# Performance work log

Measured on AMD Instinct MI355X. Metric: run time of the kernel, lower is better.

Reference implementation:

```python
import math
import jax, jax.numpy as jnp
import numpy as np

B, N, D = 4, 1024, 512
HEADS, K = 8, 3
DH = D // HEADS
SMAX, SMIN, ALPHA_S = 0.2, 0.8, 3.0


def setup_inputs() -> dict:
    key = jax.random.key(0)
    ks = jax.random.split(key, 6)
    X = jax.random.normal(ks[0], (B, N, D), dtype=jnp.float32)
    # per-head GraphConstructor temperature (init 1.0 in torch)
    temperature = jnp.ones((HEADS,), dtype=jnp.float32)
    # per-head, per-hop filter weights: [HEADS, K+1, DH, DH]
    W_filt = jax.random.normal(ks[1], (HEADS, K + 1, DH, DH), dtype=jnp.float32) / math.sqrt(DH)
    # per-head hop mixing coefficients (random so output is non-trivial)
    alpha = jax.random.normal(ks[2], (HEADS, K + 1), dtype=jnp.float32) * 0.5
    W_proj = jax.random.normal(ks[3], (D, D), dtype=jnp.float32) / math.sqrt(D)
    b_proj = jnp.zeros((D,), dtype=jnp.float32)
    return {"X": X, "temperature": temperature, "W_filt": W_filt, "alpha": alpha,
            "W_proj": W_proj, "b_proj": b_proj, "layer_idx": 1, "L": 4}


def reference(X, temperature, W_filt, alpha, W_proj, b_proj, layer_idx, L):
    b, n, d = X.shape
    Xh = X.reshape(b, n, HEADS, DH).transpose(0, 2, 1, 3)  # [B,H,N,DH]

    # sparsity schedule -> static top-k size
    sparsity = SMIN + (SMAX - SMIN) * math.exp(-ALPHA_S * layer_idx / L)
    k_val = max(1, int((1.0 - sparsity) * n))

    tau = jnp.clip(temperature, 0.1, 5.0)  # [H]
    scale = math.sqrt(DH)
    # per-head attention scores: [B,H,N,N]
    S = jnp.einsum('bhnd,bhmd->bhnm', Xh, Xh) / (scale * tau[None, :, None, None])

    if k_val < n:
        thresh = jax.lax.top_k(S, k_val)[0][..., -1:]  # k-th largest per row
        S = jnp.where(S < thresh, -jnp.inf, S)
    A = jax.nn.softmax(S, axis=-1)  # row-stochastic sparse-pattern adjacency

    # K-hop polynomial filter, all heads at once
    P = Xh
    H = alpha[None, :, 0, None, None] * jnp.einsum('bhnd,hde->bhne', P, W_filt[:, 0])
    for k in range(1, K + 1):
        P = jnp.einsum('bhnm,bhmd->bhnd', A, P)
        H = H + alpha[None, :, k, None, None] * jnp.einsum('bhnd,hde->bhne', P, W_filt[:, k])

    out = H.transpose(0, 2, 1, 3).reshape(b, n, d)  # concat heads
    return out @ W_proj.T + b_proj
```

## Files before the change

### kernel.cpp

```cpp
#include <hip/hip_runtime.h>
#include <math.h>

#define Nq   1024
#define Dq   512
#define Hq   8
#define KH   3
#define DHq  64
#define NBH  32

typedef __attribute__((ext_vector_type(8))) __bf16 bf16x8;
typedef __attribute__((ext_vector_type(4))) float f32x4;

#define LDA 136
#define LDW 72


__device__ __forceinline__ unsigned short f2bf(float f) {
    unsigned int u = __float_as_uint(f);
    u += 0x7FFFu + ((u >> 16) & 1u);
    return (unsigned short)(u >> 16);
}
__device__ __forceinline__ float bf2f(unsigned short b) {
    return __uint_as_float(((unsigned int)b) << 16);
}
__device__ __forceinline__ unsigned key16(unsigned int b) {
    return (b & 0x8000u) ? (0xFFFFu & ~b) : (b | 0x8000u);
}
__device__ __forceinline__ uint2 pack4(float4 v) {
    return make_uint2((unsigned)f2bf(v.x) | ((unsigned)f2bf(v.y) << 16),
                      (unsigned)f2bf(v.z) | ((unsigned)f2bf(v.w) << 16));
}
__device__ __forceinline__ f32x4 fzero() { f32x4 z = {0.f, 0.f, 0.f, 0.f}; return z; }



__global__ __launch_bounds__(256) void xcast_kernel(const float* __restrict__ X,
                                                    unsigned short* __restrict__ Xn,
                                                    unsigned short* __restrict__ Xt,
                                                    const float* __restrict__ Wf,
                                                    const float* __restrict__ Wp,
                                                    unsigned short* __restrict__ WtB,
                                                    unsigned short* __restrict__ WpB) {
    int tid = threadIdx.x;
    if (blockIdx.y == 32) {
        int bx = blockIdx.x;
#pragma unroll
        for (int mm = 0; mm < 2; ++mm) {
            int m = bx * 2 + mm;
            for (int u = tid; u < 4096; u += 256) {
                int d = u >> 6, e = u & 63;
                WtB[m * 4096 + e * 64 + d] = f2bf(Wf[m * 4096 + d * 64 + e]);
            }
        }
        for (int u = tid; u < 32 * 128; u += 256) {
            int r = bx * 32 + (u >> 7), c4 = (u & 127) << 2;
            float4 v = *(const float4*)&Wp[(size_t)r * Dq + c4];
            *(uint2*)&WpB[(size_t)r * Dq + c4] = pack4(v);
        }
        return;
    }
    __shared__ float T[64][68];
    int bh = blockIdx.y, b = bh >> 3, h = bh & 7;
    int n0 = blockIdx.x << 6;
    const float* Xg = X + ((size_t)b * Nq + n0) * Dq + h * DHq;
#pragma unroll
    for (int u = 0; u < 4; ++u) {
        int idx = tid + (u << 8);
        int r = idx >> 4, c4 = (idx & 15) << 2;
        float4 v = *(const float4*)&Xg[(size_t)r * Dq + c4];
        *(uint2*)&Xn[((size_t)bh * Nq + n0 + r) * DHq + c4] = pack4(v);
        T[c4 + 0][r] = v.x; T[c4 + 1][r] = v.y; T[c4 + 2][r] = v.z; T[c4 + 3][r] = v.w;
    }
    __syncthreads();
#pragma unroll
    for (int u = 0; u < 4; ++u) {
        int idx = tid + (u << 8);
        int d = idx >> 4, n4 = (idx & 15) << 2;
        float4 v = make_float4(T[d][n4], T[d][n4 + 1], T[d][n4 + 2], T[d][n4 + 3]);
        *(uint2*)&Xt[((size_t)bh * DHq + d) * Nq + n0 + n4] = pack4(v);
    }
}

__global__ __launch_bounds__(256) void score_mfma(const unsigned short* __restrict__ Xn,
                                                  const float* __restrict__ temperature,
                                                  unsigned short* __restrict__ Sbf) {
    __shared__ unsigned short Xi[64 * LDW], Xj[64 * LDW];
    int tid = threadIdx.x, lane = tid & 63, w = tid >> 6;
    int bh = blockIdx.z, i0 = blockIdx.y << 6, j0 = blockIdx.x << 6;
    const unsigned short* Xb = Xn + (size_t)bh * Nq * DHq;
    {
        int row = tid >> 3, o = (tid & 7) << 3;
#pragma unroll
        for (int u = 0; u < 2; ++u) {
            int r = row + (u << 5);
            *(uint4*)&Xi[r * LDW + o] = *(const uint4*)&Xb[(size_t)(i0 + r) * DHq + o];
            *(uint4*)&Xj[r * LDW + o] = *(const uint4*)&Xb[(size_t)(j0 + r) * DHq + o];
        }
    }
    __syncthreads();
    f32x4 acc[4] = {fzero(), fzero(), fzero(), fzero()};
    int brow = lane & 15, ko = (lane >> 4) << 3;
    const unsigned short* Afr = &Xi[((w << 4) + brow) * LDW + ko];
#pragma unroll
    for (int ks = 0; ks < 2; ++ks) {
        bf16x8 af = *(const bf16x8*)(Afr + (ks << 5));
#pragma unroll
        for (int nt = 0; nt < 4; ++nt) {
            bf16x8 bfv = *(const bf16x8*)&Xj[((nt << 4) + brow) * LDW + (ks << 5) + ko];
            acc[nt] = __builtin_amdgcn_mfma_f32_16x16x32_bf16(af, bfv, acc[nt], 0, 0, 0);
        }
    }
    float tau = fminf(fmaxf(temperature[bh & 7], 0.1f), 5.0f);
    float inv = 1.0f / (8.0f * tau);
    int nrow = (w << 4) + ((lane >> 4) << 2);
    unsigned short* Sp = Sbf + ((size_t)bh * Nq + i0 + nrow) * Nq + j0;
#pragma unroll
    for (int nt = 0; nt < 4; ++nt)
#pragma unroll
        for (int r = 0; r < 4; ++r)
            Sp[(size_t)r * Nq + (nt << 4) + brow] = f2bf(acc[nt][r] * inv);
}

__global__ __launch_bounds__(256) void topk_softmax_kernel(unsigned short* __restrict__ Sbf,
                                                           const int* __restrict__ layer_idx,
                                                           const int* __restrict__ Lptr) {
    int tid = threadIdx.x;
    int w = tid >> 6, lane = tid & 63;
    unsigned short* Srow = Sbf + ((size_t)blockIdx.x * 4 + w) * Nq;
    uint4 q0 = ((const uint4*)Srow)[lane * 2];
    uint4 q1 = ((const uint4*)Srow)[lane * 2 + 1];
    float v[16]; unsigned int k16[16];
    {
        unsigned int ww[8] = {q0.x, q0.y, q0.z, q0.w, q1.x, q1.y, q1.z, q1.w};
#pragma unroll
        for (int i = 0; i < 8; ++i) {
            unsigned lo16 = ww[i] & 0xFFFFu, hi16 = ww[i] >> 16;
            v[2 * i]       = __uint_as_float(lo16 << 16);
            v[2 * i + 1]   = __uint_as_float(hi16 << 16);
            k16[2 * i]     = key16(lo16);
            k16[2 * i + 1] = key16(hi16);
        }
    }

    double sp = 0.8 + (0.2 - 0.8) * exp(-3.0 * (double)layer_idx[0] / (double)Lptr[0]);
    int kv = (int)((1.0 - sp) * (double)Nq);
    if (kv < 1) kv = 1;

    float m = v[0];
#pragma unroll
    for (int i = 1; i < 16; ++i) m = fmaxf(m, v[i]);
#pragma unroll
    for (int off = 32; off; off >>= 1) m = fmaxf(m, __shfl_xor(m, off));
    unsigned int maxk = key16(__float_as_uint(m) >> 16);

    unsigned int tk = 0;
    if (kv < Nq) {
        unsigned int lo = 0;
#pragma unroll
        for (int bit = 15; bit >= 0; --bit) {
            unsigned int t = lo | (1u << bit);
            if (t > maxk) continue;
            int cnt = 0;
#pragma unroll
            for (int i = 0; i < 16; ++i)
                cnt += (int)__popcll(__ballot(k16[i] >= t));
            if (cnt >= kv) lo = t;
        }
        tk = lo;
    }

    float sum = 0.f;
#pragma unroll
    for (int i = 0; i < 16; ++i) {
        float e = (k16[i] >= tk) ? __expf(v[i] - m) : 0.0f;
        v[i] = e; sum += e;
    }
#pragma unroll
    for (int off = 32; off; off >>= 1) sum += __shfl_xor(sum, off);
    float is = 1.0f / sum;
    unsigned int ow[8];
#pragma unroll
    for (int i = 0; i < 8; ++i)
        ow[i] = (unsigned)f2bf(v[2 * i] * is) | ((unsigned)f2bf(v[2 * i + 1] * is) << 16);
    ((uint4*)Srow)[lane * 2]     = make_uint4(ow[0], ow[1], ow[2], ow[3]);
    ((uint4*)Srow)[lane * 2 + 1] = make_uint4(ow[4], ow[5], ow[6], ow[7]);
}

__global__ __launch_bounds__(256) void apf_mfma(const unsigned short* __restrict__ Abf,
                                                const unsigned short* __restrict__ Ptin,
                                                unsigned short* __restrict__ Ptout, int writeP,
                                                const unsigned short* __restrict__ Xn,
                                                const unsigned short* __restrict__ WtB,
                                                const float* __restrict__ alpha,
                                                unsigned short* __restrict__ HaccB, int khop) {
    __shared__ unsigned short A_lds[2][64 * LDA];
    __shared__ unsigned short P_lds[2][64 * LDA];
    int tid = threadIdx.x, lane = tid & 63, w = tid >> 6;
    int bh = blockIdx.y, b = bh >> 3, h = bh & 7;
    int i0 = blockIdx.x << 6;
    const unsigned short* Ag = Abf + ((size_t)bh * Nq + i0) * Nq;
    const unsigned short* Pg = Ptin + (size_t)bh * DHq * Nq;
    int r0 = tid >> 4, oo = (tid & 15) << 3;

    uint4 ra[4], rp[4];
#pragma unroll
    for (int u = 0; u < 4; ++u) {
        ra[u] = *(const uint4*)&Ag[(size_t)(r0 + (u << 4)) * Nq + oo];
        rp[u] = *(const uint4*)&Pg[(size_t)(r0 + (u << 4)) * Nq + oo];
    }
#pragma unroll
    for (int u = 0; u < 4; ++u) {
        *(uint4*)&A_lds[0][(r0 + (u << 4)) * LDA + oo] = ra[u];
        *(uint4*)&P_lds[0][(r0 + (u << 4)) * LDA + oo] = rp[u];
    }
    __syncthreads();

    f32x4 acc[4] = {fzero(), fzero(), fzero(), fzero()};
    int brow = lane & 15, g = lane >> 4, ko = g << 3;
    int cur = 0;

    for (int kt = 0; kt < 8; ++kt) {
        if (kt < 7) {
            int j = (kt + 1) << 7;
#pragma unroll
            for (int u = 0; u < 4; ++u) {
                ra[u] = *(const uint4*)&Ag[(size_t)(r0 + (u << 4)) * Nq + j + oo];
                rp[u] = *(const uint4*)&Pg[(size_t)(r0 + (u << 4)) * Nq + j + oo];
            }
        }
        const unsigned short* Afr = &A_lds[cur][((w << 4) + brow) * LDA + ko];
#pragma unroll
        for (int ks = 0; ks < 4; ++ks) {
            bf16x8 af = *(const bf16x8*)(Afr + (ks << 5));
#pragma unroll
            for (int nt = 0; nt < 4; ++nt) {
                bf16x8 bfv = *(const bf16x8*)&P_lds[cur][((nt << 4) + brow) * LDA + (ks << 5) + ko];
                acc[nt] = __builtin_amdgcn_mfma_f32_16x16x32_bf16(af, bfv, acc[nt], 0, 0, 0);
            }
        }
        if (kt < 7) {
#pragma unroll
            for (int u = 0; u < 4; ++u) {
                *(uint4*)&A_lds[cur ^ 1][(r0 + (u << 4)) * LDA + oo] = ra[u];
                *(uint4*)&P_lds[cur ^ 1][(r0 + (u << 4)) * LDA + oo] = rp[u];
            }
        }
        __syncthreads();
        cur ^= 1;
    }

    int nrow = (w << 4) + (g << 2);
    int dcol = brow;
    if (writeP) {
#pragma unroll
        for (int nt = 0; nt < 4; ++nt) {
            uint2 pk = make_uint2(
                (unsigned)f2bf(acc[nt][0]) | ((unsigned)f2bf(acc[nt][1]) << 16),
                (unsigned)f2bf(acc[nt][2]) | ((unsigned)f2bf(acc[nt][3]) << 16));
            *(uint2*)&Ptout[(size_t)bh * DHq * Nq + (size_t)((nt << 4) + dcol) * Nq + i0 + nrow] = pk;
        }
    }
    unsigned short* PnL = &A_lds[0][0];
#pragma unroll
    for (int nt = 0; nt < 4; ++nt)
#pragma unroll
        for (int r = 0; r < 4; ++r)
            PnL[(nrow + r) * LDW + (nt << 4) + dcol] = f2bf(acc[nt][r]);

    const unsigned short* Wk = WtB + (size_t)(h * (KH + 1) + khop) * DHq * DHq;
    f32x4 hacc[4] = {fzero(), fzero(), fzero(), fzero()};
    f32x4 hacc0[4] = {fzero(), fzero(), fzero(), fzero()};
#pragma unroll
    for (int ks = 0; ks < 2; ++ks) {
        bf16x8 pf = *(const bf16x8*)&PnL[((w << 4) + brow) * LDW + (ks << 5) + ko];
#pragma unroll
        for (int nt = 0; nt < 4; ++nt) {
            bf16x8 wf = *(const bf16x8*)&Wk[(size_t)((nt << 4) + brow) * DHq + (ks << 5) + ko];
            hacc[nt] = __builtin_amdgcn_mfma_f32_16x16x32_bf16(pf, wf, hacc[nt], 0, 0, 0);
        }
    }
    if (khop == 1) {
        const unsigned short* W0 = WtB + (size_t)(h * (KH + 1)) * DHq * DHq;
        const unsigned short* Xb = Xn + ((size_t)bh * Nq + i0) * DHq;
        int arow = (w << 4) + brow;
#pragma unroll
        for (int ks = 0; ks < 2; ++ks) {
            bf16x8 xf = *(const bf16x8*)&Xb[(size_t)arow * DHq + (ks << 5) + ko];
#pragma unroll
            for (int nt = 0; nt < 4; ++nt) {
                bf16x8 wf = *(const bf16x8*)&W0[(size_t)((nt << 4) + brow) * DHq + (ks << 5) + ko];
                hacc0[nt] = __builtin_amdgcn_mfma_f32_16x16x32_bf16(xf, wf, hacc0[nt], 0, 0, 0);
            }
        }
    }
    float av = alpha[h * (KH + 1) + khop];
    unsigned short* Ho = HaccB + ((size_t)b * Nq + i0 + nrow) * Dq + h * DHq;
    if (khop == 1) {
        float a0 = alpha[h * (KH + 1)];
#pragma unroll
        for (int nt = 0; nt < 4; ++nt)
#pragma unroll
            for (int r = 0; r < 4; ++r)
                Ho[(size_t)r * Dq + (nt << 4) + brow] = f2bf(a0 * hacc0[nt][r] + av * hacc[nt][r]);
    } else {
#pragma unroll
        for (int nt = 0; nt < 4; ++nt)
#pragma unroll
            for (int r = 0; r < 4; ++r) {
                unsigned short* p = Ho + (size_t)r * Dq + (nt << 4) + brow;
                *p = f2bf(bf2f(*p) + av * hacc[nt][r]);
            }
    }
}

__global__ __launch_bounds__(256) void proj_mfma(const unsigned short* __restrict__ HaccB,
                                                 const unsigned short* __restrict__ WpB,
                                                 const float* __restrict__ bp,
                                                 float* __restrict__ out) {
    __shared__ unsigned short Hl[64 * LDA], Wl[64 * LDA];
    int tid = threadIdx.x, lane = tid & 63, w = tid >> 6;
    int i0 = blockIdx.y << 6, j0 = blockIdx.x << 6;
    int brow = lane & 15, ko = (lane >> 4) << 3;
    f32x4 acc[4] = {fzero(), fzero(), fzero(), fzero()};
    for (int kt = 0; kt < 4; ++kt) {
#pragma unroll
        for (int u = 0; u < 4; ++u) {
            int idx = tid + (u << 8);
            int r = idx >> 4, c8 = (idx & 15) << 3;
            *(uint4*)&Hl[r * LDA + c8] = *(const uint4*)&HaccB[(size_t)(i0 + r) * Dq + (kt << 7) + c8];
            *(uint4*)&Wl[r * LDA + c8] = *(const uint4*)&WpB[(size_t)(j0 + r) * Dq + (kt << 7) + c8];
        }
        __syncthreads();
        const unsigned short* Afr = &Hl[((w << 4) + brow) * LDA + ko];
#pragma unroll
        for (int ks = 0; ks < 4; ++ks) {
            bf16x8 af = *(const bf16x8*)(Afr + (ks << 5));
#pragma unroll
            for (int nt = 0; nt < 4; ++nt) {
                bf16x8 bfv = *(const bf16x8*)&Wl[((nt << 4) + brow) * LDA + (ks << 5) + ko];
                acc[nt] = __builtin_amdgcn_mfma_f32_16x16x32_bf16(af, bfv, acc[nt], 0, 0, 0);
            }
        }
        __syncthreads();
    }
    int nrow = (w << 4) + ((lane >> 4) << 2);
#pragma unroll
    for (int nt = 0; nt < 4; ++nt) {
        float bb = bp[j0 + (nt << 4) + brow];
#pragma unroll
        for (int r = 0; r < 4; ++r)
            out[(size_t)(i0 + nrow + r) * Dq + j0 + (nt << 4) + brow] = acc[nt][r] + bb;
    }
}


extern "C" void kernel_launch(void* const* d_in, const int* in_sizes, int n_in,
                              void* d_out, int out_size, void* d_ws, size_t ws_size,
                              hipStream_t stream) {
    (void)in_sizes; (void)n_in; (void)out_size; (void)ws_size;
    const float* X           = (const float*)d_in[0];
    const float* temperature = (const float*)d_in[1];
    const float* W_filt      = (const float*)d_in[2];
    const float* alpha       = (const float*)d_in[3];
    const float* W_proj      = (const float*)d_in[4];
    const float* b_proj      = (const float*)d_in[5];
    const int*   layer_idx   = (const int*)d_in[6];
    const int*   Lp          = (const int*)d_in[7];
    float* out = (float*)d_out;

    unsigned short* Abf  = (unsigned short*)d_ws;
    unsigned short* Xn   = Abf  + (size_t)NBH * Nq * Nq;
    unsigned short* Xt   = Xn   + (size_t)NBH * Nq * DHq;
    unsigned short* Pt1  = Xt   + (size_t)NBH * DHq * Nq;
    unsigned short* Pt2  = Pt1  + (size_t)NBH * DHq * Nq;
    unsigned short* Hacc = Pt2  + (size_t)NBH * DHq * Nq;
    unsigned short* WtB  = Hacc + (size_t)4 * Nq * Dq;
    unsigned short* WpB  = WtB  + (size_t)NBH * DHq * DHq;

    dim3 blk(256);
    xcast_kernel<<<dim3(16, 33), blk, 0, stream>>>(X, Xn, Xt, W_filt, W_proj, WtB, WpB);
    score_mfma<<<dim3(16, 16, 32), blk, 0, stream>>>(Xn, temperature, Abf);
    topk_softmax_kernel<<<dim3(NBH * Nq / 4), blk, 0, stream>>>(Abf, layer_idx, Lp);

    apf_mfma<<<dim3(16, 32), blk, 0, stream>>>(Abf, Xt, Pt1, 1, Xn, WtB, alpha, Hacc, 1);
    apf_mfma<<<dim3(16, 32), blk, 0, stream>>>(Abf, Pt1, Pt2, 1, Xn, WtB, alpha, Hacc, 2);
    apf_mfma<<<dim3(16, 32), blk, 0, stream>>>(Abf, Pt2, nullptr, 0, Xn, WtB, alpha, Hacc, 3);

    proj_mfma<<<dim3(8, 64), blk, 0, stream>>>(Hacc, WpB, b_proj, out);
}
```

Measured before the change: 217.2 us.

## Stage score tile through LDS, early-exit top-k search, deepen apf prefetch

The score kernel now stages each bf16 output tile in shared memory and writes it out with 16-byte row stores instead of scattered 2-byte stores. The top-k radix search stops early once the count equals k exactly and takes the minimum qualifying key as the threshold. The A·P kernel adds a second register prefetch buffer so global loads run two tiles ahead, and fully unrolls the loop. This trades extra registers and shared memory, which can lower occupancy, for better store coalescing and more latency hiding.

After: 311.4 us. 1.43x slower.

```diff
diff --git a/kernel.cpp b/kernel.cpp
--- a/kernel.cpp
+++ b/kernel.cpp
@@ -85,6 +85,7 @@
                                                   const float* __restrict__ temperature,
                                                   unsigned short* __restrict__ Sbf) {
     __shared__ unsigned short Xi[64 * LDW], Xj[64 * LDW];
+    __shared__ unsigned short Cst[64 * 68];
     int tid = threadIdx.x, lane = tid & 63, w = tid >> 6;
     int bh = blockIdx.z, i0 = blockIdx.y << 6, j0 = blockIdx.x << 6;
     const unsigned short* Xb = Xn + (size_t)bh * Nq * DHq;
@@ -99,7 +100,7 @@
     }
     __syncthreads();
     f32x4 acc[4] = {fzero(), fzero(), fzero(), fzero()};
-    int brow = lane & 15, ko = (lane >> 4) << 3;
+    int brow = lane & 15, g = lane >> 4, ko = g << 3;
     const unsigned short* Afr = &Xi[((w << 4) + brow) * LDW + ko];
 #pragma unroll
     for (int ks = 0; ks < 2; ++ks) {
@@ -112,13 +113,19 @@
     }
     float tau = fminf(fmaxf(temperature[bh & 7], 0.1f), 5.0f);
     float inv = 1.0f / (8.0f * tau);
-    int nrow = (w << 4) + ((lane >> 4) << 2);
-    unsigned short* Sp = Sbf + ((size_t)bh * Nq + i0 + nrow) * Nq + j0;
+    int nrow = (w << 4) + (g << 2);
 #pragma unroll
     for (int nt = 0; nt < 4; ++nt)
 #pragma unroll
         for (int r = 0; r < 4; ++r)
-            Sp[(size_t)r * Nq + (nt << 4) + brow] = f2bf(acc[nt][r] * inv);
+            Cst[(nrow + r) * 68 + (nt << 4) + brow] = f2bf(acc[nt][r] * inv);
+    __syncthreads();
+    {
+        int rr = tid >> 2, c16 = (tid & 3) << 4;
+        unsigned short* Sp = Sbf + ((size_t)bh * Nq + i0 + rr) * Nq + j0 + c16;
+        *(uint4*)Sp       = *(const uint4*)&Cst[rr * 68 + c16];
+        *(uint4*)(Sp + 8) = *(const uint4*)&Cst[rr * 68 + c16 + 8];
+    }
 }
 
 __global__ __launch_bounds__(256) void topk_softmax_kernel(unsigned short* __restrict__ Sbf,
@@ -156,15 +163,30 @@
     unsigned int tk = 0;
     if (kv < Nq) {
         unsigned int lo = 0;
+        bool done = false;
 #pragma unroll
         for (int bit = 15; bit >= 0; --bit) {
+            if (done) continue;
             unsigned int t = lo | (1u << bit);
             if (t > maxk) continue;
             int cnt = 0;
 #pragma unroll
             for (int i = 0; i < 16; ++i)
                 cnt += (int)__popcll(__ballot(k16[i] >= t));
-            if (cnt >= kv) lo = t;
+            if (cnt >= kv) {
+                lo = t;
+                if (cnt == kv) {
+                    unsigned int mn = 0xFFFFu;
+#pragma unroll
+                    for (int i = 0; i < 16; ++i)
+                        mn = min(mn, (k16[i] >= t) ? k16[i] : 0xFFFFu);
+#pragma unroll
+                    for (int off = 32; off; off >>= 1)
+                        mn = min(mn, (unsigned)__shfl_xor((int)mn, off));
+                    lo = mn;
+                    done = true;
+                }
+            }
         }
         tk = lo;
     }
@@ -202,16 +224,21 @@
     const unsigned short* Pg = Ptin + (size_t)bh * DHq * Nq;
     int r0 = tid >> 4, oo = (tid & 15) << 3;
 
-    uint4 ra[4], rp[4];
+    uint4 ra[2][4], rp[2][4];
 #pragma unroll
     for (int u = 0; u < 4; ++u) {
-        ra[u] = *(const uint4*)&Ag[(size_t)(r0 + (u << 4)) * Nq + oo];
-        rp[u] = *(const uint4*)&Pg[(size_t)(r0 + (u << 4)) * Nq + oo];
+        ra[0][u] = *(const uint4*)&Ag[(size_t)(r0 + (u << 4)) * Nq + oo];
+        rp[0][u] = *(const uint4*)&Pg[(size_t)(r0 + (u << 4)) * Nq + oo];
     }
 #pragma unroll
     for (int u = 0; u < 4; ++u) {
-        *(uint4*)&A_lds[0][(r0 + (u << 4)) * LDA + oo] = ra[u];
-        *(uint4*)&P_lds[0][(r0 + (u << 4)) * LDA + oo] = rp[u];
+        *(uint4*)&A_lds[0][(r0 + (u << 4)) * LDA + oo] = ra[0][u];
+        *(uint4*)&P_lds[0][(r0 + (u << 4)) * LDA + oo] = rp[0][u];
+    }
+#pragma unroll
+    for (int u = 0; u < 4; ++u) {
+        ra[1][u] = *(const uint4*)&Ag[(size_t)(r0 + (u << 4)) * Nq + 128 + oo];
+        rp[1][u] = *(const uint4*)&Pg[(size_t)(r0 + (u << 4)) * Nq + 128 + oo];
     }
     __syncthreads();
 
@@ -219,13 +246,16 @@
     int brow = lane & 15, g = lane >> 4, ko = g << 3;
     int cur = 0;
 
+#pragma unroll
     for (int kt = 0; kt < 8; ++kt) {
-        if (kt < 7) {
-            int j = (kt + 1) << 7;
+        const int si = kt & 1;
+        const int sw = si ^ 1;
+        if (kt < 6) {
+            int j = (kt + 2) << 7;
 #pragma unroll
             for (int u = 0; u < 4; ++u) {
-                ra[u] = *(const uint4*)&Ag[(size_t)(r0 + (u << 4)) * Nq + j + oo];
-                rp[u] = *(const uint4*)&Pg[(size_t)(r0 + (u << 4)) * Nq + j + oo];
+                ra[si][u] = *(const uint4*)&Ag[(size_t)(r0 + (u << 4)) * Nq + j + oo];
+                rp[si][u] = *(const uint4*)&Pg[(size_t)(r0 + (u << 4)) * Nq + j + oo];
             }
         }
         const unsigned short* Afr = &A_lds[cur][((w << 4) + brow) * LDA + ko];
@@ -241,8 +271,8 @@
         if (kt < 7) {
 #pragma unroll
             for (int u = 0; u < 4; ++u) {
-                *(uint4*)&A_lds[cur ^ 1][(r0 + (u << 4)) * LDA + oo] = ra[u];
-                *(uint4*)&P_lds[cur ^ 1][(r0 + (u << 4)) * LDA + oo] = rp[u];
+                *(uint4*)&A_lds[cur ^ 1][(r0 + (u << 4)) * LDA + oo] = ra[sw][u];
+                *(uint4*)&P_lds[cur ^ 1][(r0 + (u << 4)) * LDA + oo] = rp[sw][u];
             }
         }
         __syncthreads();
```
